# Performance work log

Measured on AMD Instinct MI355X. Metric: run time of the kernel, lower is better.

Reference implementation:

```python
import jax, jax.numpy as jnp
import numpy as np

N_NODES = 100000
N_EDGES = 1600000
D_FEAT = 64


def setup_inputs() -> dict:
    key = jax.random.key(0)
    k1, k2 = jax.random.split(key)
    x = jax.random.normal(k1, (N_NODES, D_FEAT), dtype=jnp.float32)
    edge_index = jax.random.randint(k2, (2, N_EDGES), 0, N_NODES, dtype=jnp.int64)
    return {"x": x, "edge_index": edge_index}


def reference(x, edge_index):
    # flow='source_to_target': j = edge_index[0] (source), i = edge_index[1] (target)
    # message: x_j = gather source node features along dim 0
    msgs = x[edge_index[0]]                      # [E, D]
    # aggregate: scatter-add messages to target nodes, dim_size = N
    out = jax.ops.segment_sum(msgs, edge_index[1], num_segments=x.shape[0])  # [N, D]
    # update: identity
    return out
```

## Files before the change

### kernel.cpp

```cpp
#include <hip/hip_runtime.h>

#define D_FEAT 64
#define SUBN 128
#define SUBN_SHIFT 7
#define NBINS_MAX 1024
#define SCAN_BLOCK 256
#define SCAN_ELEMS 1024
#define SCAN_SHIFT 10

__global__ __launch_bounds__(256) void k_atomic_scatter(
    const float* __restrict__ x, const int* __restrict__ src,
    const int* __restrict__ tgt, float* __restrict__ out, int n_edges)
{
    const int lane = threadIdx.x & 63;
    const int wave = threadIdx.x >> 6;
    const int e = blockIdx.x * 4 + wave;
    if (e >= n_edges) return;
    const float v = x[(long long)src[e] * D_FEAT + lane];
    atomicAdd(&out[(long long)tgt[e] * D_FEAT + lane], v);
}

__global__ __launch_bounds__(256) void k_convert_count(
    const float* __restrict__ x, unsigned short* __restrict__ xb, int n4,
    const int* __restrict__ tgt, int* __restrict__ cnt, int E, int NBINS, int CH)
{
    __shared__ int c[NBINS_MAX];
    const int tid = threadIdx.x;
    const int stride = gridDim.x * 256;
    for (int i = blockIdx.x * 256 + tid; i < n4; i += stride) {
        float4 f = ((const float4*)x)[i];
        ushort4 u;
        unsigned int b;
        b = __float_as_uint(f.x); u.x = (unsigned short)((b + 0x7fffu + ((b >> 16) & 1u)) >> 16);
        b = __float_as_uint(f.y); u.y = (unsigned short)((b + 0x7fffu + ((b >> 16) & 1u)) >> 16);
        b = __float_as_uint(f.z); u.z = (unsigned short)((b + 0x7fffu + ((b >> 16) & 1u)) >> 16);
        b = __float_as_uint(f.w); u.w = (unsigned short)((b + 0x7fffu + ((b >> 16) & 1u)) >> 16);
        ((ushort4*)xb)[i] = u;
    }
    for (int i = tid; i < NBINS; i += 256) c[i] = 0;
    __syncthreads();
    const int base = blockIdx.x * CH;
    const int lim = min(E, base + CH);
    for (int e = base + tid; e < lim; e += 256)
        atomicAdd(&c[tgt[e] >> SUBN_SHIFT], 1);
    __syncthreads();
    for (int i = tid; i < NBINS; i += 256) cnt[(size_t)blockIdx.x * NBINS + i] = c[i];
}

__global__ __launch_bounds__(SCAN_BLOCK) void k_scan_partial_T(
    const int* __restrict__ cnt, int* __restrict__ off,
    int* __restrict__ bsum, int M, int NBINS, int NBLK)
{
    __shared__ int lds[SCAN_BLOCK];
    const int tid = threadIdx.x;
    const int base = blockIdx.x * SCAN_ELEMS + tid * 4;
    int v[4];
#pragma unroll
    for (int k = 0; k < 4; ++k) {
        int i = base + k;
        if (i < M) {
            int bin = i / NBLK;
            int blk = i - bin * NBLK;
            v[k] = cnt[(size_t)blk * NBINS + bin];
        } else v[k] = 0;
    }
    const int tsum = v[0] + v[1] + v[2] + v[3];
    int val = tsum;
    lds[tid] = val;
    __syncthreads();
    for (int d = 1; d < SCAN_BLOCK; d <<= 1) {
        int add = (tid >= d) ? lds[tid - d] : 0;
        __syncthreads();
        val += add;
        lds[tid] = val;
        __syncthreads();
    }
    if (tid == SCAN_BLOCK - 1) bsum[blockIdx.x] = val;
    int p = val - tsum;
#pragma unroll
    for (int k = 0; k < 4; ++k) {
        int i = base + k;
        if (i < M) { off[i] = p; p += v[k]; }
    }
}

__global__ __launch_bounds__(1024) void k_scan_sums(int* __restrict__ bsum, int nb)
{
    __shared__ int lds[1024];
    const int tid = threadIdx.x;
    const int v = (tid < nb) ? bsum[tid] : 0;
    int val = v;
    lds[tid] = val;
    __syncthreads();
    for (int d = 1; d < 1024; d <<= 1) {
        int add = (tid >= d) ? lds[tid - d] : 0;
        __syncthreads();
        val += add;
        lds[tid] = val;
        __syncthreads();
    }
    if (tid < nb) bsum[tid] = val - v;
}

__global__ __launch_bounds__(256) void k_bin_scatter(
    const int* __restrict__ src, const int* __restrict__ tgt,
    const int* __restrict__ off, const int* __restrict__ bsum,
    int* __restrict__ binned, int E, int NBINS, int NBLK, int CH)
{
    __shared__ int ofs[NBINS_MAX];
    const int tid = threadIdx.x;
    const int b = blockIdx.x;
    for (int i = tid; i < NBINS; i += 256) {
        size_t idx = (size_t)i * NBLK + b;
        ofs[i] = off[idx] + bsum[idx >> SCAN_SHIFT];
    }
    __syncthreads();
    const int base = b * CH;
    const int lim = min(E, base + CH);
    for (int e = base + tid; e < lim; e += 256) {
        int t = tgt[e];
        int s = src[e];
        int bin = t >> SUBN_SHIFT;
        int p = atomicAdd(&ofs[bin], 1);
        binned[p] = (s << SUBN_SHIFT) | (t & (SUBN - 1));
    }
}

__global__ __launch_bounds__(256) void k_bin_sort(
    const int* __restrict__ binned, const int* __restrict__ off,
    const int* __restrict__ bsum,
    int* __restrict__ srcSorted, int* __restrict__ nodeOff,
    int E, int N, int NBLK, int NBINS)
{
    __shared__ int hist[SUBN];
    __shared__ int ofs[SUBN];
    const int tid = threadIdx.x;
    const int bin = blockIdx.x;
    const size_t i0 = (size_t)bin * NBLK;
    const int binStart = off[i0] + bsum[i0 >> SCAN_SHIFT];
    int binEnd;
    if (bin + 1 < NBINS) {
        const size_t i1 = (size_t)(bin + 1) * NBLK;
        binEnd = off[i1] + bsum[i1 >> SCAN_SHIFT];
    } else binEnd = E;
    if (tid < SUBN) hist[tid] = 0;
    __syncthreads();
    for (int e = binStart + tid; e < binEnd; e += 256)
        atomicAdd(&hist[binned[e] & (SUBN - 1)], 1);
    __syncthreads();
    int orig = (tid < SUBN) ? hist[tid] : 0;
    int val = orig;
    if (tid < SUBN) ofs[tid] = val;
    __syncthreads();
    for (int d = 1; d < SUBN; d <<= 1) {
        int add = (tid >= d && tid < SUBN) ? ofs[tid - d] : 0;
        __syncthreads();
        if (tid < SUBN) { val += add; ofs[tid] = val; }
        __syncthreads();
    }
    if (tid < SUBN) {
        int abs0 = binStart + (val - orig);
        ofs[tid] = abs0;
        int node = bin * SUBN + tid;
        if (node < N) nodeOff[node] = abs0;
    }
    if (bin == 0 && tid == 0) nodeOff[N] = E;
    __syncthreads();
    for (int e = binStart + tid; e < binEnd; e += 256) {
        int entry = binned[e];
        int p = atomicAdd(&ofs[entry & (SUBN - 1)], 1);
        srcSorted[p] = entry >> SUBN_SHIFT;
    }
}

__global__ __launch_bounds__(256) void k_gather_bf2(
    const unsigned short* __restrict__ xb, const int* __restrict__ srcSorted,
    const int* __restrict__ nodeOff, float* __restrict__ out, int N)
{
    const int lane = threadIdx.x & 63;
    const int wave = threadIdx.x >> 6;
    const int half = lane >> 5;
    const int hl = lane & 31;
    const int wid0 = blockIdx.x * 4 + wave;
    const int wstride = gridDim.x * 4;

    for (int v = wid0; v < N; v += wstride) {
        const int start = __builtin_amdgcn_readfirstlane(nodeOff[v]);
        const int end   = __builtin_amdgcn_readfirstlane(nodeOff[v + 1]);
        float acc0 = 0.f, acc1 = 0.f;
        int k = start;
        for (; k + 16 <= end; k += 16) {
            int s[8]; unsigned int u[8];
#pragma unroll
            for (int j = 0; j < 8; ++j) s[j] = srcSorted[k + 2 * j + half];
#pragma unroll
            for (int j = 0; j < 8; ++j)
                u[j] = *(const unsigned int*)(xb + (size_t)s[j] * D_FEAT + 2 * hl);
#pragma unroll
            for (int j = 0; j < 8; ++j) {
                acc0 += __uint_as_float(u[j] << 16);
                acc1 += __uint_as_float(u[j] & 0xffff0000u);
            }
        }
        if (k + 8 <= end) {
            int s[4]; unsigned int u[4];
#pragma unroll
            for (int j = 0; j < 4; ++j) s[j] = srcSorted[k + 2 * j + half];
#pragma unroll
            for (int j = 0; j < 4; ++j)
                u[j] = *(const unsigned int*)(xb + (size_t)s[j] * D_FEAT + 2 * hl);
#pragma unroll
            for (int j = 0; j < 4; ++j) {
                acc0 += __uint_as_float(u[j] << 16);
                acc1 += __uint_as_float(u[j] & 0xffff0000u);
            }
            k += 8;
        }
        if (k + 4 <= end) {
            int s[2]; unsigned int u[2];
#pragma unroll
            for (int j = 0; j < 2; ++j) s[j] = srcSorted[k + 2 * j + half];
#pragma unroll
            for (int j = 0; j < 2; ++j)
                u[j] = *(const unsigned int*)(xb + (size_t)s[j] * D_FEAT + 2 * hl);
#pragma unroll
            for (int j = 0; j < 2; ++j) {
                acc0 += __uint_as_float(u[j] << 16);
                acc1 += __uint_as_float(u[j] & 0xffff0000u);
            }
            k += 4;
        }
        for (; k < end; k += 2) {
            int e = k + half;
            unsigned int u = 0;
            if (e < end)
                u = *(const unsigned int*)(xb + (size_t)srcSorted[e] * D_FEAT + 2 * hl);
            acc0 += __uint_as_float(u << 16);
            acc1 += __uint_as_float(u & 0xffff0000u);
        }
        acc0 += __shfl_xor(acc0, 32, 64);
        acc1 += __shfl_xor(acc1, 32, 64);
        if (half == 0)
            *(float2*)(out + (size_t)v * D_FEAT + 2 * hl) = make_float2(acc0, acc1);
    }
}

__global__ __launch_bounds__(256) void k_gather(
    const float* __restrict__ x, const int* __restrict__ srcSorted,
    const int* __restrict__ nodeOff, float* __restrict__ out, int N)
{
    const int lane = threadIdx.x & 63;
    const int wave = threadIdx.x >> 6;
    const int v = blockIdx.x * 4 + wave;
    if (v >= N) return;
    const int start = __builtin_amdgcn_readfirstlane(nodeOff[v]);
    const int end   = __builtin_amdgcn_readfirstlane(nodeOff[v + 1]);
    float acc = 0.f;
    int k = start;
    for (; k + 16 <= end; k += 16) {
        int s[16];
#pragma unroll
        for (int j = 0; j < 16; ++j) s[j] = srcSorted[k + j];
        float a[16];
#pragma unroll
        for (int j = 0; j < 16; ++j) a[j] = x[(size_t)s[j] * D_FEAT + lane];
        float t0 = (a[0]+a[1])+(a[2]+a[3]), t1 = (a[4]+a[5])+(a[6]+a[7]);
        float t2 = (a[8]+a[9])+(a[10]+a[11]), t3 = (a[12]+a[13])+(a[14]+a[15]);
        acc += (t0 + t1) + (t2 + t3);
    }
    for (; k < end; ++k)
        acc += x[(size_t)srcSorted[k] * D_FEAT + lane];
    out[(size_t)v * D_FEAT + lane] = acc;
}

static inline size_t xbf_pad(int N) {
    return ((size_t)N * D_FEAT * 2 + 255) & ~(size_t)255;
}
static inline size_t ws_need(long long M, int E, int N, int with_bf) {
    size_t b = ((size_t)2 * M + 1024 + 2 * (size_t)E + N + 1) * sizeof(int);
    if (with_bf) b += xbf_pad(N);
    return b;
}

extern "C" void kernel_launch(void* const* d_in, const int* in_sizes, int n_in,
                              void* d_out, int out_size, void* d_ws, size_t ws_size,
                              hipStream_t stream)
{
    const float* x  = (const float*)d_in[0];
    const int*   ei = (const int*)d_in[1];
    const int E = in_sizes[1] / 2;
    const int N = out_size / D_FEAT;
    const int* src = ei;
    const int* tgt = ei + E;
    float* out = (float*)d_out;

    const int NBINS = (N + SUBN - 1) / SUBN;

    int CH = 0, NBLK = 0, USE_BF = 0; long long M = 0; int nScan = 0;
    const int ch_opts[3] = {4096, 8192, 16384};
    for (int bf = 1; bf >= 0 && CH == 0; --bf) {
        for (int c = 0; c < 3; ++c) {
            int ch = ch_opts[c];
            int nblk = (E + ch - 1) / ch;
            long long m = (long long)nblk * NBINS;
            int ns = (int)((m + SCAN_ELEMS - 1) / SCAN_ELEMS);
            if (ns <= 1024 && ws_need(m, E, N, bf) <= ws_size) {
                CH = ch; NBLK = nblk; M = m; nScan = ns; USE_BF = bf; break;
            }
        }
    }

    if (CH == 0 || NBINS > NBINS_MAX || (long long)N * SUBN >= (1LL << 31)) {
        hipMemsetAsync(d_out, 0, (size_t)out_size * sizeof(float), stream);
        k_atomic_scatter<<<(E + 3) / 4, 256, 0, stream>>>(x, src, tgt, out, E);
        return;
    }

    unsigned short* xbf = (unsigned short*)d_ws;
    int* cnt = (int*)((char*)d_ws + (USE_BF ? xbf_pad(N) : 0));
    int* off = cnt + M;
    int* bsum = off + M;
    int* binned = bsum + 1024;
    int* srcSorted = binned + E;
    int* nodeOff = srcSorted + E;

    const int n4 = USE_BF ? (N * D_FEAT / 4) : 0;
    k_convert_count<<<NBLK, 256, 0, stream>>>(x, xbf, n4, tgt, cnt, E, NBINS, CH);
    k_scan_partial_T<<<nScan, SCAN_BLOCK, 0, stream>>>(cnt, off, bsum, (int)M, NBINS, NBLK);
    k_scan_sums<<<1, 1024, 0, stream>>>(bsum, nScan);
    k_bin_scatter<<<NBLK, 256, 0, stream>>>(src, tgt, off, bsum, binned, E, NBINS, NBLK, CH);
    k_bin_sort<<<NBINS, 256, 0, stream>>>(binned, off, bsum, srcSorted, nodeOff, E, N, NBLK, NBINS);
    if (USE_BF)
        k_gather_bf2<<<2048, 256, 0, stream>>>(xbf, srcSorted, nodeOff, out, N);
    else
        k_gather<<<(N + 3) / 4, 256, 0, stream>>>(x, srcSorted, nodeOff, out, N);
}
```

Measured before the change: 93.44 us.

## Fold block-sum scan into bin kernels and widen sub-bins to 256 nodes

Removes the standalone single-block scan-of-sums launch; instead each bin_scatter and bin_sort block redundantly scans the partial block sums in shared memory. Sub-bin width doubles from 128 to 256 nodes, halving the number of bins and bin_sort blocks and letting all 256 threads take part in the histogram scan. This trades one kernel launch and its serial dependency for redundant per-block scan work, and leaves fewer, larger bins with more LDS atomic contention.

Result: faster. 89.41 us, median of 2 (-4.3%).

```diff
diff --git a/kernel.cpp b/kernel.cpp
--- a/kernel.cpp
+++ b/kernel.cpp
@@ -1,8 +1,8 @@
 #include <hip/hip_runtime.h>
 
 #define D_FEAT 64
-#define SUBN 128
-#define SUBN_SHIFT 7
+#define SUBN 256
+#define SUBN_SHIFT 8
 #define NBINS_MAX 1024
 #define SCAN_BLOCK 256
 #define SCAN_ELEMS 1024
@@ -18,6 +18,34 @@
     if (e >= n_edges) return;
     const float v = x[(long long)src[e] * D_FEAT + lane];
     atomicAdd(&out[(long long)tgt[e] * D_FEAT + lane], v);
+}
+
+__device__ __forceinline__ void block_scan_bsum(
+    const int* __restrict__ bsum, int nScan, int* __restrict__ bsumEx, int* __restrict__ lds256)
+{
+    const int tid = threadIdx.x;
+    const int base4 = tid * 4;
+    int v[4];
+#pragma unroll
+    for (int k = 0; k < 4; ++k)
+        v[k] = (base4 + k < nScan) ? bsum[base4 + k] : 0;
+    const int tsum = v[0] + v[1] + v[2] + v[3];
+    int val = tsum;
+    lds256[tid] = val;
+    __syncthreads();
+    for (int d = 1; d < 256; d <<= 1) {
+        int add = (tid >= d) ? lds256[tid - d] : 0;
+        __syncthreads();
+        val += add;
+        lds256[tid] = val;
+        __syncthreads();
+    }
+    int p = val - tsum;
+#pragma unroll
+    for (int k = 0; k < 4; ++k) {
+        if (base4 + k < nScan) { bsumEx[base4 + k] = p; p += v[k]; }
+    }
+    __syncthreads();
 }
 
 __global__ __launch_bounds__(256) void k_convert_count(
@@ -84,35 +112,20 @@
     }
 }
 
-__global__ __launch_bounds__(1024) void k_scan_sums(int* __restrict__ bsum, int nb)
-{
-    __shared__ int lds[1024];
-    const int tid = threadIdx.x;
-    const int v = (tid < nb) ? bsum[tid] : 0;
-    int val = v;
-    lds[tid] = val;
-    __syncthreads();
-    for (int d = 1; d < 1024; d <<= 1) {
-        int add = (tid >= d) ? lds[tid - d] : 0;
-        __syncthreads();
-        val += add;
-        lds[tid] = val;
-        __syncthreads();
-    }
-    if (tid < nb) bsum[tid] = val - v;
-}
-
 __global__ __launch_bounds__(256) void k_bin_scatter(
     const int* __restrict__ src, const int* __restrict__ tgt,
     const int* __restrict__ off, const int* __restrict__ bsum,
-    int* __restrict__ binned, int E, int NBINS, int NBLK, int CH)
+    int* __restrict__ binned, int E, int NBINS, int NBLK, int CH, int nScan)
 {
     __shared__ int ofs[NBINS_MAX];
+    __shared__ int bsumEx[1024];
+    __shared__ int lds256[256];
     const int tid = threadIdx.x;
     const int b = blockIdx.x;
+    block_scan_bsum(bsum, nScan, bsumEx, lds256);
     for (int i = tid; i < NBINS; i += 256) {
         size_t idx = (size_t)i * NBLK + b;
-        ofs[i] = off[idx] + bsum[idx >> SCAN_SHIFT];
+        ofs[i] = off[idx] + bsumEx[idx >> SCAN_SHIFT];
     }
     __syncthreads();
     const int base = b * CH;
@@ -130,35 +143,39 @@
     const int* __restrict__ binned, const int* __restrict__ off,
     const int* __restrict__ bsum,
     int* __restrict__ srcSorted, int* __restrict__ nodeOff,
-    int E, int N, int NBLK, int NBINS)
-{
+    int E, int N, int NBLK, int NBINS, int nScan)
+{
+    __shared__ int bsumEx[1024];
+    __shared__ int lds256[256];
     __shared__ int hist[SUBN];
     __shared__ int ofs[SUBN];
     const int tid = threadIdx.x;
     const int bin = blockIdx.x;
+    block_scan_bsum(bsum, nScan, bsumEx, lds256);
     const size_t i0 = (size_t)bin * NBLK;
-    const int binStart = off[i0] + bsum[i0 >> SCAN_SHIFT];
+    const int binStart = off[i0] + bsumEx[i0 >> SCAN_SHIFT];
     int binEnd;
     if (bin + 1 < NBINS) {
         const size_t i1 = (size_t)(bin + 1) * NBLK;
-        binEnd = off[i1] + bsum[i1 >> SCAN_SHIFT];
+        binEnd = off[i1] + bsumEx[i1 >> SCAN_SHIFT];
     } else binEnd = E;
-    if (tid < SUBN) hist[tid] = 0;
+    hist[tid] = 0;
     __syncthreads();
     for (int e = binStart + tid; e < binEnd; e += 256)
         atomicAdd(&hist[binned[e] & (SUBN - 1)], 1);
     __syncthreads();
-    int orig = (tid < SUBN) ? hist[tid] : 0;
+    int orig = hist[tid];
     int val = orig;
-    if (tid < SUBN) ofs[tid] = val;
+    ofs[tid] = val;
     __syncthreads();
     for (int d = 1; d < SUBN; d <<= 1) {
-        int add = (tid >= d && tid < SUBN) ? ofs[tid - d] : 0;
-        __syncthreads();
-        if (tid < SUBN) { val += add; ofs[tid] = val; }
-        __syncthreads();
-    }
-    if (tid < SUBN) {
+        int add = (tid >= d) ? ofs[tid - d] : 0;
+        __syncthreads();
+        val += add;
+        ofs[tid] = val;
+        __syncthreads();
+    }
+    {
         int abs0 = binStart + (val - orig);
         ofs[tid] = abs0;
         int node = bin * SUBN + tid;
@@ -310,7 +327,7 @@
         }
     }
 
-    if (CH == 0 || NBINS > NBINS_MAX || (long long)N * SUBN >= (1LL << 31)) {
+    if (CH == 0 || NBINS > NBINS_MAX || (long long)N >= (1LL << (31 - SUBN_SHIFT))) {
         hipMemsetAsync(d_out, 0, (size_t)out_size * sizeof(float), stream);
         k_atomic_scatter<<<(E + 3) / 4, 256, 0, stream>>>(x, src, tgt, out, E);
         return;
@@ -327,9 +344,8 @@
     const int n4 = USE_BF ? (N * D_FEAT / 4) : 0;
     k_convert_count<<<NBLK, 256, 0, stream>>>(x, xbf, n4, tgt, cnt, E, NBINS, CH);
     k_scan_partial_T<<<nScan, SCAN_BLOCK, 0, stream>>>(cnt, off, bsum, (int)M, NBINS, NBLK);
-    k_scan_sums<<<1, 1024, 0, stream>>>(bsum, nScan);
-    k_bin_scatter<<<NBLK, 256, 0, stream>>>(src, tgt, off, bsum, binned, E, NBINS, NBLK, CH);
-    k_bin_sort<<<NBINS, 256, 0, stream>>>(binned, off, bsum, srcSorted, nodeOff, E, N, NBLK, NBINS);
+    k_bin_scatter<<<NBLK, 256, 0, stream>>>(src, tgt, off, bsum, binned, E, NBINS, NBLK, CH, nScan);
+    k_bin_sort<<<NBINS, 256, 0, stream>>>(binned, off, bsum, srcSorted, nodeOff, E, N, NBLK, NBINS, nScan);
     if (USE_BF)
         k_gather_bf2<<<2048, 256, 0, stream>>>(xbf, srcSorted, nodeOff, out, N);
     else
```
